# Kernel optimization log

Measured on AMD Instinct MI355X. Metric: run time of the kernel, lower is better.

The kernel has to match this reference:

```python
import jax, jax.numpy as jnp
import numpy as np

B = 65536
QUERY_DIM = 1024
CROSS_DIM = 1024
HEADS = 16
DIM_HEAD = 64
INNER = HEADS * DIM_HEAD  # 1024
SCALE = DIM_HEAD ** -0.5


def setup_inputs() -> dict:
    key = jax.random.key(0)
    ks = jax.random.split(key, 7)
    s_in = 1.0 / np.sqrt(QUERY_DIM)
    s_c = 1.0 / np.sqrt(CROSS_DIM)
    s_o = 1.0 / np.sqrt(INNER)
    return {
        "latent": jax.random.normal(ks[0], (B, QUERY_DIM), jnp.float32),
        "cond_latent": jax.random.normal(ks[1], (B, CROSS_DIM), jnp.float32),
        "Wq": jax.random.normal(ks[2], (INNER, QUERY_DIM), jnp.float32) * s_in,
        "Wk": jax.random.normal(ks[3], (INNER, CROSS_DIM), jnp.float32) * s_c,
        "Wv": jax.random.normal(ks[4], (INNER, CROSS_DIM), jnp.float32) * s_c,
        "Wout": jax.random.normal(ks[5], (QUERY_DIM, INNER), jnp.float32) * s_o,
        "bout": jax.random.normal(ks[6], (QUERY_DIM,), jnp.float32) * s_o,
    }


def reference(latent, cond_latent, Wq, Wk, Wv, Wout, bout):
    # projections: [B, inner] -> [B, heads, dim_head]
    Q = (latent @ Wq.T).reshape(B, HEADS, DIM_HEAD)
    K = (cond_latent @ Wk.T).reshape(B, HEADS, DIM_HEAD)
    V = (cond_latent @ Wv.T).reshape(B, HEADS, DIM_HEAD)
    # attention across the heads axis: scores [B, heads, heads]
    scores = jnp.einsum("bhd,bgd->bhg", Q, K) * SCALE
    probs = jax.nn.softmax(scores, axis=-1)
    feats = jnp.einsum("bhg,bgd->bhd", probs, V).reshape(B, INNER)
    return feats @ Wout.T + bout
```

## Files before the change

### kernel.cpp

```cpp
#include <hip/hip_runtime.h>
#include <hip/hip_bf16.h>

#define NB    65536
#define KDIM  1024
#define NDIM  1024

#define BM 256
#define BN 256
#define BK 64
#define NT (KDIM / BK)

typedef float f32x4 __attribute__((ext_vector_type(4)));
typedef short short8 __attribute__((ext_vector_type(8)));
typedef unsigned short ushort8v __attribute__((ext_vector_type(8)));

static __device__ __forceinline__ unsigned short f2bf(float f) {
    union { float f; unsigned u; } v; v.f = f;
    unsigned r = v.u + 0x7FFFu + ((v.u >> 16) & 1u);
    return (unsigned short)(r >> 16);
}
static __device__ __forceinline__ float bf2f(unsigned short h) {
    union { unsigned u; float f; } v; v.u = ((unsigned)h) << 16;
    return v.f;
}

static __device__ __forceinline__ void gload16(const unsigned short* g, unsigned short* l) {
    __builtin_amdgcn_global_load_lds(
        (const __attribute__((address_space(1))) unsigned int*)g,
        (__attribute__((address_space(3))) unsigned int*)l, 16, 0, 0);
}

__global__ __launch_bounds__(256) void f32_to_bf16_k(
    const float* __restrict__ s, unsigned short* __restrict__ d, int n4)
{
    const int stride = gridDim.x * 256;
    for (int i = blockIdx.x * 256 + threadIdx.x; i < n4; i += stride) {
        float4 v = reinterpret_cast<const float4*>(s)[i];
        ushort4 o;
        o.x = f2bf(v.x); o.y = f2bf(v.y); o.z = f2bf(v.z); o.w = f2bf(v.w);
        reinterpret_cast<ushort4*>(d)[i] = o;
    }
}

template<int OUT_F32>
__global__ __launch_bounds__(512, 2) void gemm256(
    const unsigned short* __restrict__ Ap, const unsigned short* __restrict__ Wp,
    const float* __restrict__ bias, void* __restrict__ Cptr)
{
    constexpr int N = NDIM;
    constexpr int GN = NDIM / BN;
    __shared__ alignas(16) unsigned short lds[2][2][16][1024];

    const int t    = threadIdx.x;
    const int lane = t & 63;
    const int wid  = t >> 6;
    const int wm   = wid >> 2;
    const int wn   = wid & 3;

    const int nwg  = gridDim.x;
    const int cpx  = nwg >> 3;
    const int orig = blockIdx.x;
    const int wgid = (orig & 7) * cpx + (orig >> 3);
    const int bn0  = (wgid & (GN - 1)) * BN;
    const int bm0  = (wgid / GN) * BM;

    const size_t aoff = (size_t)(lane & 15) * KDIM + (lane >> 4) * 8;

#define LDA_(BUF, MI, KS) \
    (*reinterpret_cast<const short8*>(&lds[BUF][0][wm * 8 + (MI)][(KS) * 512 + lane * 8]))
#define LDB_(BUF, NI, KS) \
    (*reinterpret_cast<const short8*>(&lds[BUF][1][wn * 4 + (NI)][(KS) * 512 + lane * 8]))

#define STAGE_(TAU, SLOT) do {                                                  \
        _Pragma("unroll")                                                       \
        for (int _ab = 0; _ab < 2; ++_ab) {                                     \
            const unsigned short* _b = _ab ? Wp : Ap;                           \
            int _r0 = _ab ? bn0 : bm0;                                          \
            _Pragma("unroll")                                                   \
            for (int _j = 0; _j < 2; ++_j) {                                    \
                int _f = wid * 2 + _j;                                          \
                _Pragma("unroll")                                               \
                for (int _ks = 0; _ks < 2; ++_ks)                               \
                    gload16(_b + (size_t)(_r0 + _f * 16) * KDIM                 \
                                + (TAU) * BK + _ks * 32 + aoff,                 \
                            &lds[SLOT][_ab][_f][_ks * 512]);                    \
            }                                                                   \
        }                                                                       \
    } while (0)

    f32x4 acc[8][4];
#pragma unroll
    for (int mi = 0; mi < 8; ++mi)
#pragma unroll
        for (int ni = 0; ni < 4; ++ni)
            acc[mi][ni] = (f32x4){0.f, 0.f, 0.f, 0.f};

    STAGE_(0, 0);
    asm volatile("s_waitcnt vmcnt(0)" ::: "memory");
    __builtin_amdgcn_s_barrier();

#pragma unroll 1
    for (int tt = 0; tt < NT; ++tt) {
        const int buf = tt & 1;
        if (tt + 1 < NT) STAGE_(tt + 1, buf ^ 1);

#pragma unroll
        for (int ks = 0; ks < 2; ++ks) {
            short8 af[8], bq[4];
#pragma unroll
            for (int mi = 0; mi < 8; ++mi) af[mi] = LDA_(buf, mi, ks);
#pragma unroll
            for (int ni = 0; ni < 4; ++ni) bq[ni] = LDB_(buf, ni, ks);
            __builtin_amdgcn_s_setprio(1);
#pragma unroll
            for (int mi = 0; mi < 8; ++mi)
#pragma unroll
                for (int ni = 0; ni < 4; ++ni)
                    acc[mi][ni] = __builtin_amdgcn_mfma_f32_16x16x32_bf16(
                        af[mi], bq[ni], acc[mi][ni], 0, 0, 0);
            __builtin_amdgcn_s_setprio(0);
        }
        asm volatile("s_waitcnt vmcnt(0)" ::: "memory");
        __builtin_amdgcn_s_barrier();
    }

    const int crow = (lane >> 4) * 4;
    const int ccol = lane & 15;

    if (OUT_F32) {
        float* Cf = (float*)Cptr;
        float* bbf = reinterpret_cast<float*>(&lds[0][0][0][0]);
        float bv[4];
#pragma unroll
        for (int ni = 0; ni < 4; ++ni)
            bv[ni] = bias[bn0 + wn * 64 + ni * 16 + ccol];
#pragma unroll
        for (int p = 0; p < 8; ++p) {
            if (wm == (p >> 2)) {
#pragma unroll
                for (int ml = 0; ml < 2; ++ml)
#pragma unroll
                    for (int ni = 0; ni < 4; ++ni)
#pragma unroll
                        for (int r = 0; r < 4; ++r)
                            bbf[(ml * 16 + crow + r) * 268 + wn * 64 + ni * 16 + ccol]
                                = acc[(p & 3) * 2 + ml][ni][r] + bv[ni];
            }
            __syncthreads();
#pragma unroll
            for (int it = 0; it < 4; ++it) {
                int lrow = wid * 4 + it;
                f32x4 v = *reinterpret_cast<const f32x4*>(&bbf[lrow * 268 + lane * 4]);
                *reinterpret_cast<f32x4*>(
                    &Cf[(size_t)(bm0 + p * 32 + lrow) * N + bn0 + lane * 4]) = v;
            }
            __syncthreads();
        }
    } else {
        unsigned short* Cb = (unsigned short*)Cptr;
        unsigned short* bb = &lds[0][0][0][0];
#pragma unroll
        for (int p = 0; p < 4; ++p) {
            if (wm == (p >> 1)) {
#pragma unroll
                for (int ml = 0; ml < 4; ++ml)
#pragma unroll
                    for (int ni = 0; ni < 4; ++ni)
#pragma unroll
                        for (int r = 0; r < 4; ++r)
                            bb[(ml * 16 + crow + r) * 264 + wn * 64 + ni * 16 + ccol]
                                = f2bf(acc[(p & 1) * 4 + ml][ni][r]);
            }
            __syncthreads();
#pragma unroll
            for (int it = 0; it < 4; ++it) {
                int lrow = wid * 8 + it * 2 + (lane >> 5);
                int lcol = (lane & 31) * 8;
                ushort8v v = *reinterpret_cast<const ushort8v*>(&bb[lrow * 264 + lcol]);
                *reinterpret_cast<ushort8v*>(
                    &Cb[(size_t)(bm0 + p * 64 + lrow) * N + bn0 + lcol]) = v;
            }
            __syncthreads();
        }
    }
#undef LDA_
#undef LDB_
#undef STAGE_
}

__global__ __launch_bounds__(256) void attn_k(
    const unsigned short* __restrict__ Qb, const unsigned short* __restrict__ Kb,
    const unsigned short* __restrict__ Vb, unsigned short* __restrict__ Fb)
{
    __shared__ alignas(16) unsigned short KL[4][1024];
    __shared__ alignas(16) unsigned short VL[4][1024];
    const int t = threadIdx.x;
    const int lane = t & 63;
    const int wid = t >> 6;
    const size_t row = (size_t)blockIdx.x * 4 + wid;
    const size_t base = row * 1024;
    const int off = lane * 16;

    ushort8v q0 = *reinterpret_cast<const ushort8v*>(&Qb[base + off]);
    ushort8v q1 = *reinterpret_cast<const ushort8v*>(&Qb[base + off + 8]);
    float qf[16];
#pragma unroll
    for (int j = 0; j < 8; ++j) { qf[j] = bf2f(q0[j]); qf[8 + j] = bf2f(q1[j]); }

    *reinterpret_cast<ushort8v*>(&KL[wid][off])     = *reinterpret_cast<const ushort8v*>(&Kb[base + off]);
    *reinterpret_cast<ushort8v*>(&KL[wid][off + 8]) = *reinterpret_cast<const ushort8v*>(&Kb[base + off + 8]);
    *reinterpret_cast<ushort8v*>(&VL[wid][off])     = *reinterpret_cast<const ushort8v*>(&Vb[base + off]);
    *reinterpret_cast<ushort8v*>(&VL[wid][off + 8]) = *reinterpret_cast<const ushort8v*>(&Vb[base + off + 8]);
    __syncthreads();

    const int sub = lane & 3;
    float s[16];
#pragma unroll
    for (int g = 0; g < 16; ++g) {
        const ushort8v k0 = *reinterpret_cast<const ushort8v*>(&KL[wid][g * 64 + sub * 16]);
        const ushort8v k1 = *reinterpret_cast<const ushort8v*>(&KL[wid][g * 64 + sub * 16 + 8]);
        float acc = 0.f;
#pragma unroll
        for (int j = 0; j < 8; ++j)
            acc += qf[j] * bf2f(k0[j]) + qf[8 + j] * bf2f(k1[j]);
        s[g] = acc;
    }
#pragma unroll
    for (int m = 1; m <= 2; m <<= 1)
#pragma unroll
        for (int g = 0; g < 16; ++g)
            s[g] += __shfl_xor(s[g], m, 64);

    float mx = s[0];
#pragma unroll
    for (int g = 1; g < 16; ++g) mx = fmaxf(mx, s[g]);
    float p[16], denom = 0.f;
#pragma unroll
    for (int g = 0; g < 16; ++g) {
        p[g] = __expf((s[g] - mx) * 0.125f);
        denom += p[g];
    }
    float inv = 1.f / denom;

    float f[16];
#pragma unroll
    for (int j = 0; j < 16; ++j) f[j] = 0.f;
#pragma unroll
    for (int g = 0; g < 16; ++g) {
        float pg = p[g] * inv;
        const ushort8v v0 = *reinterpret_cast<const ushort8v*>(&VL[wid][g * 64 + sub * 16]);
        const ushort8v v1 = *reinterpret_cast<const ushort8v*>(&VL[wid][g * 64 + sub * 16 + 8]);
#pragma unroll
        for (int j = 0; j < 8; ++j) {
            f[j]     += pg * bf2f(v0[j]);
            f[8 + j] += pg * bf2f(v1[j]);
        }
    }
    ushort8v o0, o1;
#pragma unroll
    for (int j = 0; j < 8; ++j) { o0[j] = f2bf(f[j]); o1[j] = f2bf(f[8 + j]); }
    *reinterpret_cast<ushort8v*>(&Fb[base + off])     = o0;
    *reinterpret_cast<ushort8v*>(&Fb[base + off + 8]) = o1;
}

extern "C" void kernel_launch(void* const* d_in, const int* in_sizes, int n_in,
                              void* d_out, int out_size, void* d_ws, size_t ws_size,
                              hipStream_t stream)
{
    (void)in_sizes; (void)n_in; (void)out_size; (void)ws_size;
    const float* latent = (const float*)d_in[0];
    const float* cond   = (const float*)d_in[1];
    const float* Wq     = (const float*)d_in[2];
    const float* Wk     = (const float*)d_in[3];
    const float* Wv     = (const float*)d_in[4];
    const float* Wout   = (const float*)d_in[5];
    const float* bout   = (const float*)d_in[6];
    float* out = (float*)d_out;

    char* ws = (char*)d_ws;
    const size_t MB = 1ull << 20;
    unsigned short* wqb = (unsigned short*)(ws + 0 * MB);
    unsigned short* wkb = (unsigned short*)(ws + 2 * MB);
    unsigned short* wvb = (unsigned short*)(ws + 4 * MB);
    unsigned short* wob = (unsigned short*)(ws + 6 * MB);
    unsigned short* Qb  = (unsigned short*)(ws + 8 * MB);
    unsigned short* Kbf = (unsigned short*)(ws + 8 * MB + 128 * MB);
    unsigned short* Vbf = (unsigned short*)(ws + 8 * MB + 256 * MB);
    unsigned short* Lb  = (unsigned short*)(ws + 8 * MB + 384 * MB);
    unsigned short* Cb  = (unsigned short*)(ws + 8 * MB + 512 * MB);

    const int wn4 = (KDIM * NDIM) / 4;
    f32_to_bf16_k<<<1024, 256, 0, stream>>>(Wq,   wqb, wn4);
    f32_to_bf16_k<<<1024, 256, 0, stream>>>(Wk,   wkb, wn4);
    f32_to_bf16_k<<<1024, 256, 0, stream>>>(Wv,   wvb, wn4);
    f32_to_bf16_k<<<1024, 256, 0, stream>>>(Wout, wob, wn4);

    const int an4 = (NB * KDIM) / 4;
    f32_to_bf16_k<<<4096, 256, 0, stream>>>(latent, Lb, an4);
    f32_to_bf16_k<<<4096, 256, 0, stream>>>(cond,   Cb, an4);

    const int nblk = (NB / BM) * (NDIM / BN);
    gemm256<0><<<nblk, 512, 0, stream>>>(Lb, wqb, nullptr, Qb);
    gemm256<0><<<nblk, 512, 0, stream>>>(Cb, wkb, nullptr, Kbf);
    gemm256<0><<<nblk, 512, 0, stream>>>(Cb, wvb, nullptr, Vbf);

    attn_k<<<NB / 4, 256, 0, stream>>>(Qb, Kbf, Vbf, Qb);

    gemm256<1><<<nblk, 512, 0, stream>>>(Qb, wob, bout, out);
}
```

Before: 1.069 ms.

## Deepen GEMM K-pipeline to four stages with BK=32 and partial vmcnt waits

The GEMM main loop now uses BK=32 with a four-slot LDS ring, prefetching three tiles ahead. It waits with a partial vmcnt(12) instead of draining all loads each iteration, so global-to-LDS traffic overlaps the MFMA work. Tail iterations clamp the tile index, which issues redundant loads. The epilogue writes larger chunks through LDS, using fewer passes and barriers, and each iteration now has two barriers.

```diff
diff --git a/kernel.cpp b/kernel.cpp
--- a/kernel.cpp
+++ b/kernel.cpp
@@ -7,7 +7,7 @@
 
 #define BM 256
 #define BN 256
-#define BK 64
+#define BK 32
 #define NT (KDIM / BK)
 
 typedef float f32x4 __attribute__((ext_vector_type(4)));
@@ -49,7 +49,7 @@
 {
     constexpr int N = NDIM;
     constexpr int GN = NDIM / BN;
-    __shared__ alignas(16) unsigned short lds[2][2][16][1024];
+    __shared__ alignas(16) unsigned short lds[4][2][16][512];
 
     const int t    = threadIdx.x;
     const int lane = t & 63;
@@ -66,12 +66,13 @@
 
     const size_t aoff = (size_t)(lane & 15) * KDIM + (lane >> 4) * 8;
 
-#define LDA_(BUF, MI, KS) \
-    (*reinterpret_cast<const short8*>(&lds[BUF][0][wm * 8 + (MI)][(KS) * 512 + lane * 8]))
-#define LDB_(BUF, NI, KS) \
-    (*reinterpret_cast<const short8*>(&lds[BUF][1][wn * 4 + (NI)][(KS) * 512 + lane * 8]))
+#define LDA_(S, MI) \
+    (*reinterpret_cast<const short8*>(&lds[S][0][wm * 8 + (MI)][lane * 8]))
+#define LDB_(S, NI) \
+    (*reinterpret_cast<const short8*>(&lds[S][1][wn * 4 + (NI)][lane * 8]))
 
 #define STAGE_(TAU, SLOT) do {                                                  \
+        int _tc = (TAU) < NT ? (TAU) : NT - 1;                  \
         _Pragma("unroll")                                                       \
         for (int _ab = 0; _ab < 2; ++_ab) {                                     \
             const unsigned short* _b = _ab ? Wp : Ap;                           \
@@ -79,11 +80,8 @@
             _Pragma("unroll")                                                   \
             for (int _j = 0; _j < 2; ++_j) {                                    \
                 int _f = wid * 2 + _j;                                          \
-                _Pragma("unroll")                                               \
-                for (int _ks = 0; _ks < 2; ++_ks)                               \
-                    gload16(_b + (size_t)(_r0 + _f * 16) * KDIM                 \
-                                + (TAU) * BK + _ks * 32 + aoff,                 \
-                            &lds[SLOT][_ab][_f][_ks * 512]);                    \
+                gload16(_b + (size_t)(_r0 + _f * 16) * KDIM + _tc * BK + aoff,  \
+                        &lds[SLOT][_ab][_f][0]);                                \
             }                                                                   \
         }                                                                       \
     } while (0)
@@ -95,34 +93,33 @@
         for (int ni = 0; ni < 4; ++ni)
             acc[mi][ni] = (f32x4){0.f, 0.f, 0.f, 0.f};
 
-    STAGE_(0, 0);
+    STAGE_(0, 0); STAGE_(1, 1); STAGE_(2, 2);
+
+#pragma unroll 1
+    for (int tt = 0; tt < NT; ++tt) {
+        const int slot = tt & 3;
+        STAGE_(tt + 3, (tt + 3) & 3);
+        asm volatile("s_waitcnt vmcnt(12)" ::: "memory");
+        __builtin_amdgcn_s_barrier();
+
+        short8 af[8], bq[4];
+#pragma unroll
+        for (int mi = 0; mi < 8; ++mi) af[mi] = LDA_(slot, mi);
+#pragma unroll
+        for (int ni = 0; ni < 4; ++ni) bq[ni] = LDB_(slot, ni);
+        __builtin_amdgcn_s_setprio(1);
+#pragma unroll
+        for (int mi = 0; mi < 8; ++mi)
+#pragma unroll
+            for (int ni = 0; ni < 4; ++ni)
+                acc[mi][ni] = __builtin_amdgcn_mfma_f32_16x16x32_bf16(
+                    af[mi], bq[ni], acc[mi][ni], 0, 0, 0);
+        __builtin_amdgcn_s_setprio(0);
+        __builtin_amdgcn_s_barrier();
+    }
+
     asm volatile("s_waitcnt vmcnt(0)" ::: "memory");
     __builtin_amdgcn_s_barrier();
-
-#pragma unroll 1
-    for (int tt = 0; tt < NT; ++tt) {
-        const int buf = tt & 1;
-        if (tt + 1 < NT) STAGE_(tt + 1, buf ^ 1);
-
-#pragma unroll
-        for (int ks = 0; ks < 2; ++ks) {
-            short8 af[8], bq[4];
-#pragma unroll
-            for (int mi = 0; mi < 8; ++mi) af[mi] = LDA_(buf, mi, ks);
-#pragma unroll
-            for (int ni = 0; ni < 4; ++ni) bq[ni] = LDB_(buf, ni, ks);
-            __builtin_amdgcn_s_setprio(1);
-#pragma unroll
-            for (int mi = 0; mi < 8; ++mi)
-#pragma unroll
-                for (int ni = 0; ni < 4; ++ni)
-                    acc[mi][ni] = __builtin_amdgcn_mfma_f32_16x16x32_bf16(
-                        af[mi], bq[ni], acc[mi][ni], 0, 0, 0);
-            __builtin_amdgcn_s_setprio(0);
-        }
-        asm volatile("s_waitcnt vmcnt(0)" ::: "memory");
-        __builtin_amdgcn_s_barrier();
-    }
 
     const int crow = (lane >> 4) * 4;
     const int ccol = lane & 15;
@@ -135,24 +132,24 @@
         for (int ni = 0; ni < 4; ++ni)
             bv[ni] = bias[bn0 + wn * 64 + ni * 16 + ccol];
 #pragma unroll
-        for (int p = 0; p < 8; ++p) {
-            if (wm == (p >> 2)) {
-#pragma unroll
-                for (int ml = 0; ml < 2; ++ml)
+        for (int p = 0; p < 4; ++p) {
+            if (wm == (p >> 1)) {
+#pragma unroll
+                for (int ml = 0; ml < 4; ++ml)
 #pragma unroll
                     for (int ni = 0; ni < 4; ++ni)
 #pragma unroll
                         for (int r = 0; r < 4; ++r)
                             bbf[(ml * 16 + crow + r) * 268 + wn * 64 + ni * 16 + ccol]
-                                = acc[(p & 3) * 2 + ml][ni][r] + bv[ni];
+                                = acc[(p & 1) * 4 + ml][ni][r] + bv[ni];
             }
             __syncthreads();
 #pragma unroll
-            for (int it = 0; it < 4; ++it) {
-                int lrow = wid * 4 + it;
+            for (int it = 0; it < 8; ++it) {
+                int lrow = wid * 8 + it;
                 f32x4 v = *reinterpret_cast<const f32x4*>(&bbf[lrow * 268 + lane * 4]);
                 *reinterpret_cast<f32x4*>(
-                    &Cf[(size_t)(bm0 + p * 32 + lrow) * N + bn0 + lane * 4]) = v;
+                    &Cf[(size_t)(bm0 + p * 64 + lrow) * N + bn0 + lane * 4]) = v;
             }
             __syncthreads();
         }
@@ -160,25 +157,25 @@
         unsigned short* Cb = (unsigned short*)Cptr;
         unsigned short* bb = &lds[0][0][0][0];
 #pragma unroll
-        for (int p = 0; p < 4; ++p) {
-            if (wm == (p >> 1)) {
-#pragma unroll
-                for (int ml = 0; ml < 4; ++ml)
+        for (int p = 0; p < 2; ++p) {
+            if (wm == p) {
+#pragma unroll
+                for (int ml = 0; ml < 8; ++ml)
 #pragma unroll
                     for (int ni = 0; ni < 4; ++ni)
 #pragma unroll
                         for (int r = 0; r < 4; ++r)
                             bb[(ml * 16 + crow + r) * 264 + wn * 64 + ni * 16 + ccol]
-                                = f2bf(acc[(p & 1) * 4 + ml][ni][r]);
+                                = f2bf(acc[ml][ni][r]);
             }
             __syncthreads();
 #pragma unroll
-            for (int it = 0; it < 4; ++it) {
-                int lrow = wid * 8 + it * 2 + (lane >> 5);
+            for (int it = 0; it < 8; ++it) {
+                int lrow = wid * 16 + it * 2 + (lane >> 5);
                 int lcol = (lane & 31) * 8;
                 ushort8v v = *reinterpret_cast<const ushort8v*>(&bb[lrow * 264 + lcol]);
                 *reinterpret_cast<ushort8v*>(
-                    &Cb[(size_t)(bm0 + p * 64 + lrow) * N + bn0 + lcol]) = v;
+                    &Cb[(size_t)(bm0 + p * 128 + lrow) * N + bn0 + lcol]) = v;
             }
             __syncthreads();
         }
```

After: 1.028 ms. 1.04x faster.
